# Kernel optimization log

Measured on AMD Instinct MI355X. Metric: run time of the kernel, lower is better.

Reference implementation:

```python
import jax, jax.numpy as jnp
import numpy as np

N_NODES = 100000
N_EDGES = 1600000
NEG_SLOPE = 0.2  # PyG GATConv default


def setup_inputs() -> dict:
    key = jax.random.key(0)
    ks = jax.random.split(key, 10)
    return {
        "x": jax.random.normal(ks[0], (N_NODES, 128), dtype=jnp.float32),
        "edge_index": jax.random.randint(ks[1], (2, N_EDGES), 0, N_NODES, dtype=jnp.int64),
        "W1": jax.random.normal(ks[2], (128, 128), dtype=jnp.float32) * 0.1,
        "a_src1": jax.random.normal(ks[3], (4, 32), dtype=jnp.float32) * 0.1,
        "a_dst1": jax.random.normal(ks[4], (4, 32), dtype=jnp.float32) * 0.1,
        "b1": jax.random.normal(ks[5], (128,), dtype=jnp.float32) * 0.1,
        "W2": jax.random.normal(ks[6], (128, 16), dtype=jnp.float32) * 0.1,
        "a_src2": jax.random.normal(ks[7], (1, 16), dtype=jnp.float32) * 0.1,
        "a_dst2": jax.random.normal(ks[8], (1, 16), dtype=jnp.float32) * 0.1,
        "b2": jax.random.normal(ks[9], (16,), dtype=jnp.float32) * 0.1,
    }


def _gat_layer(x, src, dst, W, a_src, a_dst, b, heads):
    # PyG GATConv (concat=True): xw -> per-edge attention -> segment softmax over
    # incoming edges of each target node -> weighted scatter-sum.
    N = x.shape[0]
    H = heads
    C = W.shape[1] // H
    xw = (x @ W).reshape(N, H, C)                      # [N,H,C]
    al = (xw * a_src).sum(-1)                          # [N,H] source term
    ar = (xw * a_dst).sum(-1)                          # [N,H] target term
    e = jax.nn.leaky_relu(al[src] + ar[dst], NEG_SLOPE)  # [E',H]
    emax = jax.ops.segment_max(e, dst, num_segments=N)   # [N,H]
    em = jnp.exp(e - emax[dst])
    denom = jax.ops.segment_sum(em, dst, num_segments=N)
    alpha = em / denom[dst]                            # [E',H]
    out = jax.ops.segment_sum(xw[src] * alpha[:, :, None], dst, num_segments=N)
    return out.reshape(N, H * C) + b


def reference(x, edge_index, W1, a_src1, a_dst1, b1, W2, a_src2, a_dst2, b2):
    N = x.shape[0]
    loop = jnp.arange(N, dtype=edge_index.dtype)
    # PyG GATConv add_self_loops=True
    src = jnp.concatenate([edge_index[0], loop])
    dst = jnp.concatenate([edge_index[1], loop])
    h = jax.nn.relu(_gat_layer(x, src, dst, W1, a_src1, a_dst1, b1, 4))
    # F.dropout(p=0.5, training=self.training): identity in eval mode
    return _gat_layer(h, src, dst, W2, a_src2, a_dst2, b2, 1)
```

## Files before the change

### kernel.cpp

```cpp
#include <hip/hip_runtime.h>
#include <hip/hip_fp16.h>

#define N_NODES 100000
#define N_EDGES 1600000
#define E_TOT   (N_EDGES + N_NODES)
#define NEG_SLOPE 0.2f
#define PART_EPB 4096
#define BSTRIDE 18432
#define NGEMM (N_NODES / 32)
#define NPART ((E_TOT + PART_EPB - 1) / PART_EPB)

using f16x8 = __attribute__((ext_vector_type(8))) _Float16;
using f32x4 = __attribute__((ext_vector_type(4))) float;
union H8 { f16x8 v; _Float16 h[8]; __half2 h2[4]; };

__global__ __launch_bounds__(256)
void k_gemm1_part(const float* __restrict__ x, const float* __restrict__ W1,
                  const float* __restrict__ a_src1, const float* __restrict__ a_dst1,
                  const int* __restrict__ ei, int* __restrict__ bcnt, int* __restrict__ pairs,
                  __half* __restrict__ xw1h, float* __restrict__ al1, float* __restrict__ ar1) {
    __shared__ int lcnt[128];
    __shared__ int lbase[128];
    const int t = threadIdx.x;

    if (blockIdx.x >= NGEMM) {
        const int base = ((int)blockIdx.x - NGEMM) * PART_EPB;
        if (t < 128) lcnt[t] = 0;
        __syncthreads();
        int sr[16], dr[16];
#pragma unroll
        for (int u = 0; u < 16; ++u) {
            const int e = base + u * 256 + t;
            if (e < E_TOT) {
                int s, d;
                if (e < N_EDGES) { s = ei[e]; d = ei[N_EDGES + e]; }
                else             { s = d = e - N_EDGES; }
                sr[u] = s; dr[u] = d;
                atomicAdd(&lcnt[d >> 10], 1);
            } else dr[u] = -1;
        }
        __syncthreads();
        if (t < 128) {
            const int c = lcnt[t];
            lbase[t] = (c > 0) ? atomicAdd(&bcnt[t], c) : 0;
            lcnt[t] = 0;
        }
        __syncthreads();
#pragma unroll
        for (int u = 0; u < 16; ++u) {
            if (dr[u] >= 0) {
                const int bk = dr[u] >> 10;
                const int r = atomicAdd(&lcnt[bk], 1);
                pairs[(size_t)bk * BSTRIDE + lbase[bk] + r] = (sr[u] << 10) | (dr[u] & 1023);
            }
        }
        return;
    }

    const int lane = t & 63;
    const int w = t >> 6;
    const int q = lane >> 4;
    const int n15 = lane & 15;
    const int n0 = (int)blockIdx.x * 32;
    const int j0 = (2 * w) * 16 + n15;
    const int j1 = (2 * w + 1) * 16 + n15;

    f32x4 acc00 = {0.f, 0.f, 0.f, 0.f};
    f32x4 acc01 = acc00, acc10 = acc00, acc11 = acc00;

    for (int kt = 0; kt < 4; ++kt) {
        const int k0 = kt * 32 + q * 8;
        H8 A0, A1, B0, B1;
        {
            const float4* p = (const float4*)&x[(size_t)(n0 + n15) * 128 + k0];
            const float4 xa = p[0], xb = p[1];
            A0.h2[0] = __float22half2_rn(make_float2(xa.x, xa.y));
            A0.h2[1] = __float22half2_rn(make_float2(xa.z, xa.w));
            A0.h2[2] = __float22half2_rn(make_float2(xb.x, xb.y));
            A0.h2[3] = __float22half2_rn(make_float2(xb.z, xb.w));
        }
        {
            const float4* p = (const float4*)&x[(size_t)(n0 + 16 + n15) * 128 + k0];
            const float4 xa = p[0], xb = p[1];
            A1.h2[0] = __float22half2_rn(make_float2(xa.x, xa.y));
            A1.h2[1] = __float22half2_rn(make_float2(xa.z, xa.w));
            A1.h2[2] = __float22half2_rn(make_float2(xb.x, xb.y));
            A1.h2[3] = __float22half2_rn(make_float2(xb.z, xb.w));
        }
        {
            float w0[8], w1[8];
#pragma unroll
            for (int i = 0; i < 8; ++i) {
                w0[i] = W1[(size_t)(k0 + i) * 128 + j0];
                w1[i] = W1[(size_t)(k0 + i) * 128 + j1];
            }
#pragma unroll
            for (int i = 0; i < 4; ++i) {
                B0.h2[i] = __float22half2_rn(make_float2(w0[2 * i], w0[2 * i + 1]));
                B1.h2[i] = __float22half2_rn(make_float2(w1[2 * i], w1[2 * i + 1]));
            }
        }
        acc00 = __builtin_amdgcn_mfma_f32_16x16x32_f16(A0.v, B0.v, acc00, 0, 0, 0);
        acc01 = __builtin_amdgcn_mfma_f32_16x16x32_f16(A0.v, B1.v, acc01, 0, 0, 0);
        acc10 = __builtin_amdgcn_mfma_f32_16x16x32_f16(A1.v, B0.v, acc10, 0, 0, 0);
        acc11 = __builtin_amdgcn_mfma_f32_16x16x32_f16(A1.v, B1.v, acc11, 0, 0, 0);
    }

    const float as0 = a_src1[j0], as1 = a_src1[j1];
    const float ad0 = a_dst1[j0], ad1 = a_dst1[j1];
#pragma unroll
    for (int ng = 0; ng < 2; ++ng) {
        const f32x4 accA = ng ? acc10 : acc00;
        const f32x4 accB = ng ? acc11 : acc01;
#pragma unroll
        for (int r = 0; r < 4; ++r) {
            const int node = n0 + ng * 16 + q * 4 + r;
            xw1h[(size_t)node * 128 + j0] = __float2half(accA[r]);
            xw1h[(size_t)node * 128 + j1] = __float2half(accB[r]);
            float ps = accA[r] * as0 + accB[r] * as1;
            float pd = accA[r] * ad0 + accB[r] * ad1;
#pragma unroll
            for (int o = 1; o < 16; o <<= 1) {
                ps += __shfl_xor(ps, o, 64);
                pd += __shfl_xor(pd, o, 64);
            }
            if (n15 == 0) {
                al1[(size_t)node * 4 + w] = ps;
                ar1[(size_t)node * 4 + w] = pd;
            }
        }
    }
}

__global__ __launch_bounds__(1024)
void k_fill3(const int* __restrict__ pairs, const int* __restrict__ bcnt,
             int* __restrict__ ioff, int* __restrict__ deg, int* __restrict__ ssrc) {
    const int bucket = blockIdx.x;
    const int t = threadIdx.x;
    const int cnt = bcnt[bucket];
    __shared__ int lhist[1024];
    __shared__ int lcur[1024];
    __shared__ int wsum[16];
    __shared__ int sbc[128];
    __shared__ int sbase;
    lhist[t] = 0;
    if (t < 128) sbc[t] = bcnt[t];
    __syncthreads();
    if (t == 0) {
        int b = 0;
        for (int k = 0; k < bucket; ++k) b += sbc[k];
        sbase = b;
    }
    for (int i = t; i < cnt; i += 1024) {
        const int p = pairs[(size_t)bucket * BSTRIDE + i];
        atomicAdd(&lhist[p & 1023], 1);
    }
    __syncthreads();
    const int v = lhist[t];
    int inc = v;
    const int lane = t & 63, wid = t >> 6;
#pragma unroll
    for (int o = 1; o < 64; o <<= 1) {
        const int nv = __shfl_up(inc, o, 64);
        if (lane >= o) inc += nv;
    }
    if (lane == 63) wsum[wid] = inc;
    __syncthreads();
    if (t == 0) {
        int acc = 0;
#pragma unroll
        for (int k = 0; k < 16; ++k) { const int tv = wsum[k]; wsum[k] = acc; acc += tv; }
    }
    __syncthreads();
    const int gofs = sbase + (inc - v) + wsum[wid];
    const int d = bucket * 1024 + t;
    if (d < N_NODES) { ioff[d] = gofs; deg[d] = v; }
    lcur[t] = gofs;
    __syncthreads();
    for (int i = t; i < cnt; i += 1024) {
        const int p = pairs[(size_t)bucket * BSTRIDE + i];
        const int pos = atomicAdd(&lcur[p & 1023], 1);
        ssrc[pos] = p >> 10;
    }
}

__global__ __launch_bounds__(256)
void k_aggr1(const int* __restrict__ ssrc, const int* __restrict__ offs,
             const int* __restrict__ deg, const float* __restrict__ al1,
             const float* __restrict__ ar1, const __half* __restrict__ xw1h,
             const float* __restrict__ b1, __half* __restrict__ out1h) {
    const int lane = threadIdx.x & 63;
    const int d = blockIdx.x * 4 + (threadIdx.x >> 6);
    const int g = lane >> 4;
    const int c = lane & 15;
    const int h = c >> 2;
    const int beg = offs[d];
    const int n = deg[d];
    const float arh = ar1[(size_t)d * 4 + h];
    float acc[8] = {0.f, 0.f, 0.f, 0.f, 0.f, 0.f, 0.f, 0.f};
    float dnm = 0.f;

    for (int base = 0; base < n; base += 16) {
#pragma unroll
        for (int u = 0; u < 4; ++u) {
            const int e = base + u * 4 + g;
            const bool p = e < n;
            const int s = ssrc[beg + (p ? e : 0)];
            float v = al1[(size_t)s * 4 + h] + arh;
            v = v > 0.f ? v : NEG_SLOPE * v;
            const float w = p ? __expf(v) : 0.f;
            const uint4 rv = *(const uint4*)&xw1h[(size_t)s * 128 + c * 8];
            const float2 f0 = __half22float2(*(const __half2*)&rv.x);
            const float2 f1 = __half22float2(*(const __half2*)&rv.y);
            const float2 f2 = __half22float2(*(const __half2*)&rv.z);
            const float2 f3 = __half22float2(*(const __half2*)&rv.w);
            acc[0] = fmaf(w, f0.x, acc[0]); acc[1] = fmaf(w, f0.y, acc[1]);
            acc[2] = fmaf(w, f1.x, acc[2]); acc[3] = fmaf(w, f1.y, acc[3]);
            acc[4] = fmaf(w, f2.x, acc[4]); acc[5] = fmaf(w, f2.y, acc[5]);
            acc[6] = fmaf(w, f3.x, acc[6]); acc[7] = fmaf(w, f3.y, acc[7]);
            dnm += w;
        }
    }
#pragma unroll
    for (int i = 0; i < 8; ++i) {
        acc[i] += __shfl_xor(acc[i], 16, 64);
        acc[i] += __shfl_xor(acc[i], 32, 64);
    }
    dnm += __shfl_xor(dnm, 16, 64);
    dnm += __shfl_xor(dnm, 32, 64);
    if (g == 0) {
        const float rc = 1.f / dnm;
        const float4 b01 = *(const float4*)&b1[c * 8];
        const float4 b23 = *(const float4*)&b1[c * 8 + 4];
        const float bb[8] = {b01.x, b01.y, b01.z, b01.w, b23.x, b23.y, b23.z, b23.w};
        __half ho[8];
#pragma unroll
        for (int i = 0; i < 8; ++i) {
            const float hv = acc[i] * rc + bb[i];
            ho[i] = __float2half(hv > 0.f ? hv : 0.f);
        }
        *(uint4*)&out1h[(size_t)d * 128 + c * 8] = *(uint4*)ho;
    }
}

__global__ __launch_bounds__(256)
void k_gemm2m(const __half* __restrict__ out1h, const float* __restrict__ W2,
              const float* __restrict__ a_src2, const float* __restrict__ a_dst2,
              __half* __restrict__ xw2h, float* __restrict__ al2, float* __restrict__ ar2) {
    const int t = threadIdx.x;
    const int lane = t & 63;
    const int w = t >> 6;
    const int q = lane >> 4;
    const int n15 = lane & 15;
    const int n0 = (int)blockIdx.x * 64 + w * 16;
    const int ra = n0 + n15;
    const size_t rowA = (ra < N_NODES) ? (size_t)ra : (size_t)(N_NODES - 1);

    f32x4 acc = {0.f, 0.f, 0.f, 0.f};
#pragma unroll
    for (int kt = 0; kt < 4; ++kt) {
        const int k0 = kt * 32 + q * 8;
        H8 A, B;
        A.v = *(const f16x8*)&out1h[rowA * 128 + k0];
        float wv[8];
#pragma unroll
        for (int i = 0; i < 8; ++i)
            wv[i] = W2[(size_t)(k0 + i) * 16 + n15];
#pragma unroll
        for (int i = 0; i < 4; ++i)
            B.h2[i] = __float22half2_rn(make_float2(wv[2 * i], wv[2 * i + 1]));
        acc = __builtin_amdgcn_mfma_f32_16x16x32_f16(A.v, B.v, acc, 0, 0, 0);
    }

    const float as = a_src2[n15], ad = a_dst2[n15];
#pragma unroll
    for (int r = 0; r < 4; ++r) {
        const int node = n0 + q * 4 + r;
        float ps = acc[r] * as;
        float pd = acc[r] * ad;
#pragma unroll
        for (int o = 1; o < 16; o <<= 1) {
            ps += __shfl_xor(ps, o, 64);
            pd += __shfl_xor(pd, o, 64);
        }
        if (node < N_NODES) {
            xw2h[(size_t)node * 16 + n15] = __float2half(acc[r]);
            if (n15 == 0) { al2[node] = ps; ar2[node] = pd; }
        }
    }
}

__global__ __launch_bounds__(256)
void k_aggr2(const int* __restrict__ ssrc, const int* __restrict__ offs,
             const int* __restrict__ deg, const float* __restrict__ al2,
             const float* __restrict__ ar2, const __half* __restrict__ xw2h,
             const float* __restrict__ b2, float* __restrict__ out) {
    const int lane = threadIdx.x & 63;
    const int node = blockIdx.x * 4 + (threadIdx.x >> 6);
    const int j2 = lane & 7;
    const int eL = lane >> 3;
    const int beg = offs[node];
    const int n = deg[node];
    const float ard = ar2[node];
    float a0 = 0.f, a1 = 0.f, dnm = 0.f;
    for (int base = 0; base < n; base += 32) {
#pragma unroll
        for (int u = 0; u < 4; ++u) {
            const int e = base + u * 8 + eL;
            const bool p = e < n;
            const int s = ssrc[beg + (p ? e : 0)];
            float v = al2[s] + ard;
            v = v > 0.f ? v : NEG_SLOPE * v;
            const float w = p ? __expf(v) : 0.f;
            const float2 f = __half22float2(*(const __half2*)&xw2h[(size_t)s * 16 + j2 * 2]);
            a0 = fmaf(w, f.x, a0);
            a1 = fmaf(w, f.y, a1);
            dnm += w;
        }
    }
#pragma unroll
    for (int o = 8; o < 64; o <<= 1) {
        a0 += __shfl_xor(a0, o, 64);
        a1 += __shfl_xor(a1, o, 64);
        dnm += __shfl_xor(dnm, o, 64);
    }
    if (eL == 0) {
        out[(size_t)node * 16 + j2 * 2]     = a0 / dnm + b2[j2 * 2];
        out[(size_t)node * 16 + j2 * 2 + 1] = a1 / dnm + b2[j2 * 2 + 1];
    }
}

extern "C" void kernel_launch(void* const* d_in, const int* in_sizes, int n_in,
                              void* d_out, int out_size, void* d_ws, size_t ws_size,
                              hipStream_t stream) {
    const float* x      = (const float*)d_in[0];
    const int*   ei     = (const int*)d_in[1];
    const float* W1     = (const float*)d_in[2];
    const float* a_src1 = (const float*)d_in[3];
    const float* a_dst1 = (const float*)d_in[4];
    const float* b1     = (const float*)d_in[5];
    const float* W2     = (const float*)d_in[6];
    const float* a_src2 = (const float*)d_in[7];
    const float* a_dst2 = (const float*)d_in[8];
    const float* b2     = (const float*)d_in[9];
    float* out = (float*)d_out;

    char* wsb = (char*)d_ws;
    __half* xw1h = (__half*)wsb;
    __half* xw2h = (__half*)wsb;
    float*  al2  = (float*)(wsb + (size_t)N_NODES * 16 * 2);
    float*  ar2  = al2 + N_NODES;
    __half* out1h = (__half*)(wsb + (size_t)N_NODES * 128 * 2);
    int*    pairs = (int*)out1h;
    float*  al1  = (float*)(wsb + (size_t)N_NODES * 128 * 4);
    float*  ar1  = al1 + (size_t)N_NODES * 4;
    int* ibcnt = (int*)(ar1 + (size_t)N_NODES * 4);
    int* ioff  = ibcnt + 128;
    int* ideg  = ioff + N_NODES;
    int* isrc  = ideg + N_NODES;

    hipMemsetAsync(ibcnt, 0, 128 * sizeof(int), stream);

    k_gemm1_part<<<NGEMM + NPART, 256, 0, stream>>>(x, W1, a_src1, a_dst1,
                                                    ei, ibcnt, pairs, xw1h, al1, ar1);
    k_fill3<<<128, 1024, 0, stream>>>(pairs, ibcnt, ioff, ideg, isrc);

    k_aggr1<<<N_NODES / 4, 256, 0, stream>>>(isrc, ioff, ideg, al1, ar1, xw1h, b1, out1h);

    k_gemm2m<<<(N_NODES + 63) / 64, 256, 0, stream>>>(out1h, W2, a_src2, a_dst2, xw2h, al2, ar2);

    k_aggr2<<<N_NODES / 4, 256, 0, stream>>>(isrc, ioff, ideg, al2, ar2, xw2h, b2, out);
}
```

Baseline: 309.9 us.

## Stage x tile in LDS with 64-row GEMM tiles, widen gemm2 tiles, shrink aggr1 unroll

The layer-1 GEMM now converts a 64-row tile of x to fp16 in shared memory with coalesced loads, and each wave computes four 16-row MFMA tiles. This halves the number of GEMM blocks and the redundant W1 loads, with bounds guards added for the tail. Layer-2 GEMM blocks now cover 128 rows, two MFMA tiles per wave, so each W2 fragment is reused twice. The aggr1 inner loop unroll drops from 4 to 2 edge groups per iteration, which lowers register pressure but gives less memory-level parallelism. The new 64x136 fp16 shared array is declared in the combined kernel, so it also takes LDS in the partition blocks and may lower occupancy there.

```diff
diff --git a/kernel.cpp b/kernel.cpp
--- a/kernel.cpp
+++ b/kernel.cpp
@@ -7,12 +7,13 @@
 #define NEG_SLOPE 0.2f
 #define PART_EPB 4096
 #define BSTRIDE 18432
-#define NGEMM (N_NODES / 32)
+#define NGEMM ((N_NODES + 63) / 64)
 #define NPART ((E_TOT + PART_EPB - 1) / PART_EPB)
 
 using f16x8 = __attribute__((ext_vector_type(8))) _Float16;
 using f32x4 = __attribute__((ext_vector_type(4))) float;
 union H8 { f16x8 v; _Float16 h[8]; __half2 h2[4]; };
+union H4 { __half2 h2[2]; uint2 u; };
 
 __global__ __launch_bounds__(256)
 void k_gemm1_part(const float* __restrict__ x, const float* __restrict__ W1,
@@ -21,6 +22,7 @@
                   __half* __restrict__ xw1h, float* __restrict__ al1, float* __restrict__ ar1) {
     __shared__ int lcnt[128];
     __shared__ int lbase[128];
+    __shared__ _Float16 sx[64][136];
     const int t = threadIdx.x;
 
     if (blockIdx.x >= NGEMM) {
@@ -57,36 +59,36 @@
         return;
     }
 
+    const int n0 = (int)blockIdx.x * 64;
+
+    for (int i = t; i < 64 * 32; i += 256) {
+        const int row = i >> 5;
+        const int c4 = (i & 31) * 4;
+        const int gr = n0 + row;
+        const float4 xv = *(const float4*)&x[(size_t)(gr < N_NODES ? gr : N_NODES - 1) * 128 + c4];
+        H4 tmp;
+        tmp.h2[0] = __float22half2_rn(make_float2(xv.x, xv.y));
+        tmp.h2[1] = __float22half2_rn(make_float2(xv.z, xv.w));
+        *(uint2*)&sx[row][c4] = tmp.u;
+    }
+    __syncthreads();
+
     const int lane = t & 63;
     const int w = t >> 6;
     const int q = lane >> 4;
     const int n15 = lane & 15;
-    const int n0 = (int)blockIdx.x * 32;
     const int j0 = (2 * w) * 16 + n15;
     const int j1 = (2 * w + 1) * 16 + n15;
 
-    f32x4 acc00 = {0.f, 0.f, 0.f, 0.f};
-    f32x4 acc01 = acc00, acc10 = acc00, acc11 = acc00;
+    f32x4 acc[4][2] = {};
 
     for (int kt = 0; kt < 4; ++kt) {
         const int k0 = kt * 32 + q * 8;
-        H8 A0, A1, B0, B1;
-        {
-            const float4* p = (const float4*)&x[(size_t)(n0 + n15) * 128 + k0];
-            const float4 xa = p[0], xb = p[1];
-            A0.h2[0] = __float22half2_rn(make_float2(xa.x, xa.y));
-            A0.h2[1] = __float22half2_rn(make_float2(xa.z, xa.w));
-            A0.h2[2] = __float22half2_rn(make_float2(xb.x, xb.y));
-            A0.h2[3] = __float22half2_rn(make_float2(xb.z, xb.w));
-        }
-        {
-            const float4* p = (const float4*)&x[(size_t)(n0 + 16 + n15) * 128 + k0];
-            const float4 xa = p[0], xb = p[1];
-            A1.h2[0] = __float22half2_rn(make_float2(xa.x, xa.y));
-            A1.h2[1] = __float22half2_rn(make_float2(xa.z, xa.w));
-            A1.h2[2] = __float22half2_rn(make_float2(xb.x, xb.y));
-            A1.h2[3] = __float22half2_rn(make_float2(xb.z, xb.w));
-        }
+        H8 A0, A1, A2, A3, B0, B1;
+        A0.v = *(const f16x8*)&sx[n15][k0];
+        A1.v = *(const f16x8*)&sx[16 + n15][k0];
+        A2.v = *(const f16x8*)&sx[32 + n15][k0];
+        A3.v = *(const f16x8*)&sx[48 + n15][k0];
         {
             float w0[8], w1[8];
 #pragma unroll
@@ -100,31 +102,37 @@
                 B1.h2[i] = __float22half2_rn(make_float2(w1[2 * i], w1[2 * i + 1]));
             }
         }
-        acc00 = __builtin_amdgcn_mfma_f32_16x16x32_f16(A0.v, B0.v, acc00, 0, 0, 0);
-        acc01 = __builtin_amdgcn_mfma_f32_16x16x32_f16(A0.v, B1.v, acc01, 0, 0, 0);
-        acc10 = __builtin_amdgcn_mfma_f32_16x16x32_f16(A1.v, B0.v, acc10, 0, 0, 0);
-        acc11 = __builtin_amdgcn_mfma_f32_16x16x32_f16(A1.v, B1.v, acc11, 0, 0, 0);
+        acc[0][0] = __builtin_amdgcn_mfma_f32_16x16x32_f16(A0.v, B0.v, acc[0][0], 0, 0, 0);
+        acc[0][1] = __builtin_amdgcn_mfma_f32_16x16x32_f16(A0.v, B1.v, acc[0][1], 0, 0, 0);
+        acc[1][0] = __builtin_amdgcn_mfma_f32_16x16x32_f16(A1.v, B0.v, acc[1][0], 0, 0, 0);
+        acc[1][1] = __builtin_amdgcn_mfma_f32_16x16x32_f16(A1.v, B1.v, acc[1][1], 0, 0, 0);
+        acc[2][0] = __builtin_amdgcn_mfma_f32_16x16x32_f16(A2.v, B0.v, acc[2][0], 0, 0, 0);
+        acc[2][1] = __builtin_amdgcn_mfma_f32_16x16x32_f16(A2.v, B1.v, acc[2][1], 0, 0, 0);
+        acc[3][0] = __builtin_amdgcn_mfma_f32_16x16x32_f16(A3.v, B0.v, acc[3][0], 0, 0, 0);
+        acc[3][1] = __builtin_amdgcn_mfma_f32_16x16x32_f16(A3.v, B1.v, acc[3][1], 0, 0, 0);
     }
 
     const float as0 = a_src1[j0], as1 = a_src1[j1];
     const float ad0 = a_dst1[j0], ad1 = a_dst1[j1];
 #pragma unroll
-    for (int ng = 0; ng < 2; ++ng) {
-        const f32x4 accA = ng ? acc10 : acc00;
-        const f32x4 accB = ng ? acc11 : acc01;
+    for (int m = 0; m < 4; ++m) {
 #pragma unroll
         for (int r = 0; r < 4; ++r) {
-            const int node = n0 + ng * 16 + q * 4 + r;
-            xw1h[(size_t)node * 128 + j0] = __float2half(accA[r]);
-            xw1h[(size_t)node * 128 + j1] = __float2half(accB[r]);
-            float ps = accA[r] * as0 + accB[r] * as1;
-            float pd = accA[r] * ad0 + accB[r] * ad1;
+            const int node = n0 + m * 16 + q * 4 + r;
+            const float vA = acc[m][0][r], vB = acc[m][1][r];
+            const bool ok = node < N_NODES;
+            if (ok) {
+                xw1h[(size_t)node * 128 + j0] = __float2half(vA);
+                xw1h[(size_t)node * 128 + j1] = __float2half(vB);
+            }
+            float ps = vA * as0 + vB * as1;
+            float pd = vA * ad0 + vB * ad1;
 #pragma unroll
             for (int o = 1; o < 16; o <<= 1) {
                 ps += __shfl_xor(ps, o, 64);
                 pd += __shfl_xor(pd, o, 64);
             }
-            if (n15 == 0) {
+            if (n15 == 0 && ok) {
                 al1[(size_t)node * 4 + w] = ps;
                 ar1[(size_t)node * 4 + w] = pd;
             }
@@ -200,9 +208,9 @@
     float acc[8] = {0.f, 0.f, 0.f, 0.f, 0.f, 0.f, 0.f, 0.f};
     float dnm = 0.f;
 
-    for (int base = 0; base < n; base += 16) {
-#pragma unroll
-        for (int u = 0; u < 4; ++u) {
+    for (int base = 0; base < n; base += 8) {
+#pragma unroll
+        for (int u = 0; u < 2; ++u) {
             const int e = base + u * 4 + g;
             const bool p = e < n;
             const int s = ssrc[beg + (p ? e : 0)];
@@ -252,16 +260,19 @@
     const int w = t >> 6;
     const int q = lane >> 4;
     const int n15 = lane & 15;
-    const int n0 = (int)blockIdx.x * 64 + w * 16;
-    const int ra = n0 + n15;
-    const size_t rowA = (ra < N_NODES) ? (size_t)ra : (size_t)(N_NODES - 1);
-
-    f32x4 acc = {0.f, 0.f, 0.f, 0.f};
+    const int n0 = (int)blockIdx.x * 128 + w * 16;
+    const int ra0 = n0 + n15;
+    const int ra1 = n0 + 64 + n15;
+    const size_t rowA0 = (ra0 < N_NODES) ? (size_t)ra0 : (size_t)(N_NODES - 1);
+    const size_t rowA1 = (ra1 < N_NODES) ? (size_t)ra1 : (size_t)(N_NODES - 1);
+
+    f32x4 acc0 = {0.f, 0.f, 0.f, 0.f}, acc1 = acc0;
 #pragma unroll
     for (int kt = 0; kt < 4; ++kt) {
         const int k0 = kt * 32 + q * 8;
-        H8 A, B;
-        A.v = *(const f16x8*)&out1h[rowA * 128 + k0];
+        H8 A0, A1, B;
+        A0.v = *(const f16x8*)&out1h[rowA0 * 128 + k0];
+        A1.v = *(const f16x8*)&out1h[rowA1 * 128 + k0];
         float wv[8];
 #pragma unroll
         for (int i = 0; i < 8; ++i)
@@ -269,23 +280,28 @@
 #pragma unroll
         for (int i = 0; i < 4; ++i)
             B.h2[i] = __float22half2_rn(make_float2(wv[2 * i], wv[2 * i + 1]));
-        acc = __builtin_amdgcn_mfma_f32_16x16x32_f16(A.v, B.v, acc, 0, 0, 0);
+        acc0 = __builtin_amdgcn_mfma_f32_16x16x32_f16(A0.v, B.v, acc0, 0, 0, 0);
+        acc1 = __builtin_amdgcn_mfma_f32_16x16x32_f16(A1.v, B.v, acc1, 0, 0, 0);
     }
 
     const float as = a_src2[n15], ad = a_dst2[n15];
 #pragma unroll
-    for (int r = 0; r < 4; ++r) {
-        const int node = n0 + q * 4 + r;
-        float ps = acc[r] * as;
-        float pd = acc[r] * ad;
-#pragma unroll
-        for (int o = 1; o < 16; o <<= 1) {
-            ps += __shfl_xor(ps, o, 64);
-            pd += __shfl_xor(pd, o, 64);
-        }
-        if (node < N_NODES) {
-            xw2h[(size_t)node * 16 + n15] = __float2half(acc[r]);
-            if (n15 == 0) { al2[node] = ps; ar2[node] = pd; }
+    for (int m = 0; m < 2; ++m) {
+        const f32x4 acc = m ? acc1 : acc0;
+#pragma unroll
+        for (int r = 0; r < 4; ++r) {
+            const int node = n0 + m * 64 + q * 4 + r;
+            float ps = acc[r] * as;
+            float pd = acc[r] * ad;
+#pragma unroll
+            for (int o = 1; o < 16; o <<= 1) {
+                ps += __shfl_xor(ps, o, 64);
+                pd += __shfl_xor(pd, o, 64);
+            }
+            if (node < N_NODES) {
+                xw2h[(size_t)node * 16 + n15] = __float2half(acc[r]);
+                if (n15 == 0) { al2[node] = ps; ar2[node] = pd; }
+            }
         }
     }
 }
@@ -367,7 +383,7 @@
 
     k_aggr1<<<N_NODES / 4, 256, 0, stream>>>(isrc, ioff, ideg, al1, ar1, xw1h, b1, out1h);
 
-    k_gemm2m<<<(N_NODES + 63) / 64, 256, 0, stream>>>(out1h, W2, a_src2, a_dst2, xw2h, al2, ar2);
+    k_gemm2m<<<(N_NODES + 127) / 128, 256, 0, stream>>>(out1h, W2, a_src2, a_dst2, xw2h, al2, ar2);
 
     k_aggr2<<<N_NODES / 4, 256, 0, stream>>>(isrc, ioff, ideg, al2, ar2, xw2h, b2, out);
 }
```

Measured after the change: 298.7 us. -3.6%, faster.
